# Kernel optimization log

Hardware: AMD Instinct MI355X
Metric: run time of the kernel (lower is better)

Reference implementation:

```python
import jax, jax.numpy as jnp
import numpy as np

N = 20000      # nodes (B in the original code)
T = 8          # timesteps
D_IN = 256     # in_dim (must equal hid_dim due to conv_h_n reuse in original)
D_HID = 256
D_OUT = 64
E = 320000     # edges


def setup_inputs() -> dict:
    key = jax.random.key(0)
    ks = jax.random.split(key, 18)
    s = 0.05
    w = lambda k, shape: jax.random.normal(k, shape, jnp.float32) * s
    return {
        "x": jax.random.normal(ks[0], (N, T, D_IN), jnp.float32),
        "edge_index": jax.random.randint(ks[1], (2, E), 0, N),
        "W_xr": w(ks[2], (D_IN, D_HID)),  "b_xr": w(ks[3], (D_HID,)),
        "W_hr": w(ks[4], (D_HID, D_HID)), "b_hr": w(ks[5], (D_HID,)),
        "W_xz": w(ks[6], (D_IN, D_HID)),  "b_xz": w(ks[7], (D_HID,)),
        "W_hz": w(ks[8], (D_HID, D_HID)), "b_hz": w(ks[9], (D_HID,)),
        "W_hn": w(ks[10], (D_HID, D_HID)), "b_hn": w(ks[11], (D_HID,)),
        "W_fc": w(ks[12], (D_HID, D_OUT)), "b_fc": w(ks[13], (D_OUT,)),
    }


def reference(x, edge_index, W_xr, b_xr, W_hr, b_hr, W_xz, b_xz, W_hz, b_hz,
              W_hn, b_hn, W_fc, b_fc):
    n_nodes = x.shape[0]
    src, dst = edge_index[0], edge_index[1]

    # GCN symmetric normalization with self-loops (PyG GCNConv default):
    # deg[i] = 1 + #incoming edges; norm_e = d^-1/2[src]*d^-1/2[dst]
    deg = jax.ops.segment_sum(jnp.ones(src.shape[0], x.dtype), dst,
                              num_segments=n_nodes) + jnp.asarray(1.0, x.dtype)
    dis = jax.lax.rsqrt(deg)
    enorm = dis[src] * dis[dst]      # [E]
    snorm = dis * dis                # self-loop coefficient 1/deg, [N]

    def gcn(v, W, b):
        vw = v @ W                                              # [N, D]
        agg = jax.ops.segment_sum(vw[src] * enorm[:, None], dst,
                                  num_segments=n_nodes)
        return agg + vw * snorm[:, None] + b

    def step(h, x_t):
        r = jax.nn.sigmoid(gcn(x_t, W_xr, b_xr) + gcn(h, W_hr, b_hr))
        z = jax.nn.sigmoid(gcn(x_t, W_xz, b_xz) + gcn(h, W_hz, b_hz))
        # faithful to original: conv_h_n is applied to BOTH x and h
        n = jnp.tanh(gcn(x_t, W_hn, b_hn) + r * gcn(h, W_hn, b_hn))
        h_new = (1.0 - z) * h + z * n
        return h_new, None

    h0 = jnp.zeros((n_nodes, W_hr.shape[0]), x.dtype)
    h, _ = jax.lax.scan(step, h0, jnp.transpose(x, (1, 0, 2)))  # scan over T
    return h @ W_fc + b_fc
```

## Files before the change

kernel.cpp:

```cpp
#include <hip/hip_runtime.h>
#include <hip/hip_bf16.h>
#include <math.h>

#define N_NODES 20000
#define T_STEPS 8
#define DDIM    256
#define DOUT    64
#define NE      320000
#define XSTR    2048

typedef unsigned short u16;
typedef __attribute__((ext_vector_type(8))) short  short8;
typedef __attribute__((ext_vector_type(4))) float  f32x4;

__device__ __forceinline__ float bf2f(u16 u) {
    union { unsigned int i; float f; } v; v.i = ((unsigned int)u) << 16; return v.f;
}
__device__ __forceinline__ u16 f2bf(float f) {
    union { float f; unsigned int i; } v; v.f = f;
    unsigned int r = v.i + 0x7fff + ((v.i >> 16) & 1);
    return (u16)(r >> 16);
}

__global__ void k_count(const int* __restrict__ dst, int* __restrict__ cnt) {
    int e = blockIdx.x * blockDim.x + threadIdx.x;
    if (e < NE) atomicAdd(&cnt[dst[e]], 1);
}

__global__ void k_degnorm(const int* __restrict__ cnt, float* __restrict__ dis,
                          float* __restrict__ snorm) {
    int n = blockIdx.x * blockDim.x + threadIdx.x;
    if (n < N_NODES) {
        float deg = (float)(cnt[n] + 1);
        dis[n]   = rsqrtf(deg);
        snorm[n] = 1.0f / deg;
    }
}

__global__ void k_scan(const int* __restrict__ cnt, int* __restrict__ rowptr) {
    __shared__ int sums[256];
    const int CH = (N_NODES + 255) / 256;
    int t = threadIdx.x;
    int beg = t * CH;
    int end = beg + CH; if (end > N_NODES) end = N_NODES;
    int s = 0;
    for (int i = beg; i < end; i++) s += cnt[i];
    sums[t] = s;
    __syncthreads();
    if (t == 0) {
        int run = 0;
        for (int i = 0; i < 256; i++) { int v = sums[i]; sums[i] = run; run += v; }
    }
    __syncthreads();
    if (beg < N_NODES) {
        int run = sums[t];
        for (int i = beg; i < end; i++) { rowptr[i] = run; run += cnt[i]; }
        if (end == N_NODES) rowptr[N_NODES] = run;
    }
}

__global__ void k_fill(const int* __restrict__ src, const int* __restrict__ dst,
                       const int* __restrict__ rowptr, int* __restrict__ cursor,
                       const float* __restrict__ dis, int* __restrict__ csr_src,
                       float* __restrict__ csr_norm) {
    int e = blockIdx.x * blockDim.x + threadIdx.x;
    if (e < NE) {
        int d = dst[e], s = src[e];
        int pos = atomicAdd(&cursor[d], 1);
        int i = rowptr[d] + pos;
        if (i < NE) {
            csr_src[i]  = s;
            csr_norm[i] = dis[s] * dis[d];
        }
    }
}

__global__ void k_pack6(const float* __restrict__ Wxr, const float* __restrict__ Wxz,
                        const float* __restrict__ Whn, const float* __restrict__ Whr,
                        const float* __restrict__ Whz, u16* __restrict__ out) {
    int i = blockIdx.x * blockDim.x + threadIdx.x;
    if (i >= 4 * 6 * 64 * 256) return;
    int k    = i & 255;
    int c    = (i >> 8) & 63;
    int tile = (i >> 14) % 6;
    int by   = i / (6 * 64 * 256);
    const float* W;
    switch (tile) {
        case 0: W = Wxr; break; case 1: W = Wxz; break; case 2: W = Whn; break;
        case 3: W = Whr; break; case 4: W = Whz; break; default: W = Whn; break;
    }
    out[i] = f2bf(W[k * DDIM + by * 64 + c]);
}
__global__ void k_packb3(const float* __restrict__ bxr, const float* __restrict__ bhr,
                         const float* __restrict__ bxz, const float* __restrict__ bhz,
                         const float* __restrict__ bhn, float* __restrict__ bout) {
    int c = blockIdx.x * blockDim.x + threadIdx.x;
    if (c < 3 * DDIM) {
        float v;
        if (c < 256)      v = bxr[c] + bhr[c];
        else if (c < 512) v = bxz[c - 256] + bhz[c - 256];
        else              v = bhn[c - 512];
        bout[c] = v;
    }
}

__global__ __launch_bounds__(256) void k_x2bf_all(const float* __restrict__ x,
                                                  u16* __restrict__ out) {
    int i = blockIdx.x * blockDim.x + threadIdx.x;
    if (i >= N_NODES * 512) return;
    size_t o = (size_t)i << 2;
    float4 v = *(const float4*)(x + o);
    ushort4 u; u.x = f2bf(v.x); u.y = f2bf(v.y); u.z = f2bf(v.z); u.w = f2bf(v.w);
    *(ushort4*)(out + o) = u;
}

__global__ __launch_bounds__(256) void k_agg_x(const u16* __restrict__ xall,
                      const int* __restrict__ rowptr, const int* __restrict__ csr_src,
                      const float* __restrict__ csr_norm, const float* __restrict__ snorm,
                      u16* __restrict__ xaall) {
    int n = blockIdx.x * 4 + (threadIdx.x >> 6);
    if (n >= N_NODES) return;
    int lane = threadIdx.x & 63;
    int c4 = lane << 2;
    float sn = snorm[n];
    float acc[8][4];
    const u16* selfp = xall + (size_t)n * XSTR + c4;
#pragma unroll
    for (int t = 0; t < 8; t++) {
        ushort4 v = *(const ushort4*)(selfp + t * DDIM);
        acc[t][0] = bf2f(v.x) * sn; acc[t][1] = bf2f(v.y) * sn;
        acc[t][2] = bf2f(v.z) * sn; acc[t][3] = bf2f(v.w) * sn;
    }
    int beg = rowptr[n], end = rowptr[n + 1];
    int i = beg;
    for (; i + 1 < end; i += 2) {
        const u16* sp0 = xall + (size_t)csr_src[i] * XSTR + c4;
        const u16* sp1 = xall + (size_t)csr_src[i + 1] * XSTR + c4;
        float w0 = csr_norm[i], w1 = csr_norm[i + 1];
        ushort4 g0[8], g1[8];
#pragma unroll
        for (int t = 0; t < 8; t++) g0[t] = *(const ushort4*)(sp0 + t * DDIM);
#pragma unroll
        for (int t = 0; t < 8; t++) g1[t] = *(const ushort4*)(sp1 + t * DDIM);
#pragma unroll
        for (int t = 0; t < 8; t++) {
            acc[t][0] = fmaf(bf2f(g0[t].x), w0, fmaf(bf2f(g1[t].x), w1, acc[t][0]));
            acc[t][1] = fmaf(bf2f(g0[t].y), w0, fmaf(bf2f(g1[t].y), w1, acc[t][1]));
            acc[t][2] = fmaf(bf2f(g0[t].z), w0, fmaf(bf2f(g1[t].z), w1, acc[t][2]));
            acc[t][3] = fmaf(bf2f(g0[t].w), w0, fmaf(bf2f(g1[t].w), w1, acc[t][3]));
        }
    }
    if (i < end) {
        const u16* sp = xall + (size_t)csr_src[i] * XSTR + c4;
        float w = csr_norm[i];
#pragma unroll
        for (int t = 0; t < 8; t++) {
            ushort4 g = *(const ushort4*)(sp + t * DDIM);
            acc[t][0] = fmaf(bf2f(g.x), w, acc[t][0]);
            acc[t][1] = fmaf(bf2f(g.y), w, acc[t][1]);
            acc[t][2] = fmaf(bf2f(g.z), w, acc[t][2]);
            acc[t][3] = fmaf(bf2f(g.w), w, acc[t][3]);
        }
    }
    u16* op = xaall + (size_t)n * XSTR + c4;
#pragma unroll
    for (int t = 0; t < 8; t++) {
        ushort4 o;
        o.x = f2bf(acc[t][0]); o.y = f2bf(acc[t][1]);
        o.z = f2bf(acc[t][2]); o.w = f2bf(acc[t][3]);
        *(ushort4*)(op + t * DDIM) = o;
    }
}

__global__ __launch_bounds__(256) void k_agg_bf(const u16* __restrict__ in,
                      const int* __restrict__ rowptr, const int* __restrict__ csr_src,
                      const float* __restrict__ csr_norm, const float* __restrict__ snorm,
                      u16* __restrict__ out) {
    int n = blockIdx.x * 4 + (threadIdx.x >> 6);
    if (n >= N_NODES) return;
    int lane = threadIdx.x & 63;
    int c4 = lane << 2;
    float sn = snorm[n];
    ushort4 v = *(const ushort4*)(in + (size_t)n * DDIM + c4);
    float a0 = bf2f(v.x) * sn, a1 = bf2f(v.y) * sn, a2 = bf2f(v.z) * sn, a3 = bf2f(v.w) * sn;
    int beg = rowptr[n], end = rowptr[n + 1];
    int i = beg;
    for (; i + 1 < end; i += 2) {
        ushort4 g0 = *(const ushort4*)(in + (size_t)csr_src[i] * DDIM + c4);
        ushort4 g1 = *(const ushort4*)(in + (size_t)csr_src[i + 1] * DDIM + c4);
        float w0 = csr_norm[i], w1 = csr_norm[i + 1];
        a0 = fmaf(bf2f(g0.x), w0, fmaf(bf2f(g1.x), w1, a0));
        a1 = fmaf(bf2f(g0.y), w0, fmaf(bf2f(g1.y), w1, a1));
        a2 = fmaf(bf2f(g0.z), w0, fmaf(bf2f(g1.z), w1, a2));
        a3 = fmaf(bf2f(g0.w), w0, fmaf(bf2f(g1.w), w1, a3));
    }
    if (i < end) {
        ushort4 g = *(const ushort4*)(in + (size_t)csr_src[i] * DDIM + c4);
        float w = csr_norm[i];
        a0 = fmaf(bf2f(g.x), w, a0); a1 = fmaf(bf2f(g.y), w, a1);
        a2 = fmaf(bf2f(g.z), w, a2); a3 = fmaf(bf2f(g.w), w, a3);
    }
    ushort4 o; o.x = f2bf(a0); o.y = f2bf(a1); o.z = f2bf(a2); o.w = f2bf(a3);
    *(ushort4*)(out + (size_t)n * DDIM + c4) = o;
}

__device__ __forceinline__ float sigm(float x) { return 1.0f / (1.0f + expf(-x)); }

__global__ __launch_bounds__(256) void k_gate_gru(const u16* __restrict__ xa, int ldax,
        const u16* __restrict__ ha, const u16* __restrict__ BTpack,
        const float* __restrict__ bias3, float* __restrict__ h, u16* __restrict__ hbf,
        int M) {
    __shared__ u16 Axs[64 * 32];
    __shared__ u16 Ahs[64 * 32];
    __shared__ u16 Bs[6 * 64 * 32];
    int tid = threadIdx.x;
    int w = tid >> 6, lane = tid & 63;
    int rowBase = blockIdx.x * 64;
    int by = blockIdx.y;

    int srow  = lane >> 2;
    int chunk = (lane & 3) ^ ((lane >> 3) & 3);
    int sege  = chunk * 8;
    int arow = rowBase + w * 16 + srow;
    if (arow > M - 1) arow = M - 1;
    size_t xoff = (size_t)arow * ldax + sege;
    size_t hoff = (size_t)arow * DDIM + sege;
    u16* ldsAx = &Axs[w * 16 * 32];
    u16* ldsAh = &Ahs[w * 16 * 32];
    const u16* Bbase = BTpack + (size_t)by * (6 * 64 * 256);

    f32x4 ar[2][2], az[2][2], anx[2][2], anh[2][2];
#pragma unroll
    for (int m = 0; m < 2; m++)
#pragma unroll
        for (int n = 0; n < 2; n++) {
            ar[m][n] = (f32x4){0.f,0.f,0.f,0.f}; az[m][n] = (f32x4){0.f,0.f,0.f,0.f};
            anx[m][n] = (f32x4){0.f,0.f,0.f,0.f}; anh[m][n] = (f32x4){0.f,0.f,0.f,0.f};
        }

    int kq = lane >> 4, lr = lane & 15;
    int kqs = (kq ^ ((lr >> 1) & 3)) << 3;

    for (int k0 = 0; k0 < DDIM; k0 += 32) {
        __builtin_amdgcn_global_load_lds(
            (const __attribute__((address_space(1))) void*)(xa + xoff + k0),
            (__attribute__((address_space(3))) void*)ldsAx, 16, 0, 0);
        __builtin_amdgcn_global_load_lds(
            (const __attribute__((address_space(1))) void*)(ha + hoff + k0),
            (__attribute__((address_space(3))) void*)ldsAh, 16, 0, 0);
#pragma unroll
        for (int j6 = 0; j6 < 6; j6++) {
            int j = w * 6 + j6;
            int tile = j >> 2, q = j & 3;
            const u16* src = Bbase + ((size_t)tile * 64 + q * 16 + srow) * 256 + k0 + sege;
            u16* dst = &Bs[tile * 2048 + q * 512];
            __builtin_amdgcn_global_load_lds(
                (const __attribute__((address_space(1))) void*)src,
                (__attribute__((address_space(3))) void*)dst, 16, 0, 0);
        }
        __syncthreads();

        short8 ax[2], ah[2], bf[6][2];
#pragma unroll
        for (int m = 0; m < 2; m++) {
            int r = (w >> 1) * 32 + m * 16 + lr;
            ax[m] = *(const short8*)&Axs[r * 32 + kqs];
            ah[m] = *(const short8*)&Ahs[r * 32 + kqs];
        }
#pragma unroll
        for (int t = 0; t < 6; t++)
#pragma unroll
            for (int n = 0; n < 2; n++) {
                int c = (w & 1) * 32 + n * 16 + lr;
                bf[t][n] = *(const short8*)&Bs[t * 2048 + c * 32 + kqs];
            }
#pragma unroll
        for (int m = 0; m < 2; m++)
#pragma unroll
            for (int n = 0; n < 2; n++) {
                ar[m][n]  = __builtin_amdgcn_mfma_f32_16x16x32_bf16(ax[m], bf[0][n], ar[m][n], 0, 0, 0);
                ar[m][n]  = __builtin_amdgcn_mfma_f32_16x16x32_bf16(ah[m], bf[3][n], ar[m][n], 0, 0, 0);
                az[m][n]  = __builtin_amdgcn_mfma_f32_16x16x32_bf16(ax[m], bf[1][n], az[m][n], 0, 0, 0);
                az[m][n]  = __builtin_amdgcn_mfma_f32_16x16x32_bf16(ah[m], bf[4][n], az[m][n], 0, 0, 0);
                anx[m][n] = __builtin_amdgcn_mfma_f32_16x16x32_bf16(ax[m], bf[2][n], anx[m][n], 0, 0, 0);
                anh[m][n] = __builtin_amdgcn_mfma_f32_16x16x32_bf16(ah[m], bf[5][n], anh[m][n], 0, 0, 0);
            }
        __syncthreads();
    }

#pragma unroll
    for (int n = 0; n < 2; n++) {
        int col = by * 64 + (w & 1) * 32 + n * 16 + lr;
        float br = bias3[col], bz = bias3[256 + col], bn = bias3[512 + col];
#pragma unroll
        for (int m = 0; m < 2; m++) {
            int row0 = rowBase + (w >> 1) * 32 + m * 16 + kq * 4;
#pragma unroll
            for (int j = 0; j < 4; j++) {
                int row = row0 + j;
                if (row < M) {
                    float r = sigm(ar[m][n][j] + br);
                    float z = sigm(az[m][n][j] + bz);
                    float nn = tanhf(anx[m][n][j] + bn + r * (anh[m][n][j] + bn));
                    size_t idx = (size_t)row * DDIM + col;
                    float hv = h[idx];
                    hv = (1.0f - z) * hv + z * nn;
                    h[idx] = hv;
                    hbf[idx] = f2bf(hv);
                }
            }
        }
    }
}

__global__ __launch_bounds__(256) void k_gemm(const float* __restrict__ A,
        const float* __restrict__ B, const float* __restrict__ bias,
        float* __restrict__ C, int M, int N, int K) {
    __shared__ float Asm[16][132];
    __shared__ float Bsm[16][128];
    int tid = threadIdx.x;
    int tx = tid & 15, ty = tid >> 4;
    int rowBase = blockIdx.x * 128;
    int colBase = blockIdx.y * 128;

    float acc[8][8];
#pragma unroll
    for (int i = 0; i < 8; i++)
#pragma unroll
        for (int j = 0; j < 8; j++) acc[i][j] = 0.0f;

    int arow = tid >> 1;
    int acol = (tid & 1) * 8;
    int brow = tid >> 4;
    int bcol = (tid & 15) * 8;

    bool avalid = (rowBase + arow) < M;
    const float* Aptr = A + (size_t)(rowBase + arow) * K + acol;
    int bc = colBase + bcol;
    bool bvalid = bc < N;

    for (int k0 = 0; k0 < K; k0 += 16) {
        float4 a0 = {0,0,0,0}, a1 = {0,0,0,0};
        if (avalid) {
            a0 = *(const float4*)(Aptr + k0);
            a1 = *(const float4*)(Aptr + k0 + 4);
        }
        Asm[acol + 0][arow] = a0.x; Asm[acol + 1][arow] = a0.y;
        Asm[acol + 2][arow] = a0.z; Asm[acol + 3][arow] = a0.w;
        Asm[acol + 4][arow] = a1.x; Asm[acol + 5][arow] = a1.y;
        Asm[acol + 6][arow] = a1.z; Asm[acol + 7][arow] = a1.w;

        float4 b0 = {0,0,0,0}, b1 = {0,0,0,0};
        if (bvalid) {
            const float* Bp = B + (size_t)(k0 + brow) * N + bc;
            b0 = *(const float4*)(Bp);
            b1 = *(const float4*)(Bp + 4);
        }
        *(float4*)&Bsm[brow][bcol]     = b0;
        *(float4*)&Bsm[brow][bcol + 4] = b1;
        __syncthreads();

#pragma unroll
        for (int k = 0; k < 16; k++) {
            float a[8], b[8];
            *(float4*)&a[0] = *(const float4*)&Asm[k][ty * 8];
            *(float4*)&a[4] = *(const float4*)&Asm[k][ty * 8 + 4];
            *(float4*)&b[0] = *(const float4*)&Bsm[k][tx * 8];
            *(float4*)&b[4] = *(const float4*)&Bsm[k][tx * 8 + 4];
#pragma unroll
            for (int i = 0; i < 8; i++)
#pragma unroll
                for (int j = 0; j < 8; j++)
                    acc[i][j] = fmaf(a[i], b[j], acc[i][j]);
        }
        __syncthreads();
    }

    int c0 = colBase + tx * 8;
    if (c0 < N) {
        float4 bia0 = *(const float4*)(bias + c0);
        float4 bia1 = *(const float4*)(bias + c0 + 4);
#pragma unroll
        for (int i = 0; i < 8; i++) {
            int r = rowBase + ty * 8 + i;
            if (r < M) {
                float4 o0, o1;
                o0.x = acc[i][0] + bia0.x; o0.y = acc[i][1] + bia0.y;
                o0.z = acc[i][2] + bia0.z; o0.w = acc[i][3] + bia0.w;
                o1.x = acc[i][4] + bia1.x; o1.y = acc[i][5] + bia1.y;
                o1.z = acc[i][6] + bia1.z; o1.w = acc[i][7] + bia1.w;
                *(float4*)(C + (size_t)r * N + c0)     = o0;
                *(float4*)(C + (size_t)r * N + c0 + 4) = o1;
            }
        }
    }
}

extern "C" void kernel_launch(void* const* d_in, const int* in_sizes, int n_in,
                              void* d_out, int out_size, void* d_ws, size_t ws_size,
                              hipStream_t stream) {
    const float* x    = (const float*)d_in[0];
    const int*   eidx = (const int*)d_in[1];
    const int*   src  = eidx;
    const int*   dst  = eidx + NE;
    const float* W_xr = (const float*)d_in[2];  const float* b_xr = (const float*)d_in[3];
    const float* W_hr = (const float*)d_in[4];  const float* b_hr = (const float*)d_in[5];
    const float* W_xz = (const float*)d_in[6];  const float* b_xz = (const float*)d_in[7];
    const float* W_hz = (const float*)d_in[8];  const float* b_hz = (const float*)d_in[9];
    const float* W_hn = (const float*)d_in[10]; const float* b_hn = (const float*)d_in[11];
    const float* W_fc = (const float*)d_in[12]; const float* b_fc = (const float*)d_in[13];
    float* out = (float*)d_out;

    char* ws = (char*)d_ws;
    size_t off = 0;
    auto alloc = [&](size_t bytes) -> char* {
        char* p = ws + off;
        off += (bytes + 255) & ~(size_t)255;
        return p;
    };
    const size_t NB  = (size_t)N_NODES * DDIM * 4;
    const size_t NBH = (size_t)N_NODES * DDIM * 2;
    u16*   xall    = (u16*)alloc((size_t)N_NODES * XSTR * 2);
    u16*   xaall   = (u16*)alloc((size_t)N_NODES * XSTR * 2);
    float* h       = (float*)alloc(NB);
    u16*   hbf     = (u16*)alloc(NBH);
    u16*   ha      = (u16*)alloc(NBH);
    u16*   BTpack  = (u16*)alloc((size_t)4 * 6 * 64 * 256 * 2);
    float* bias3   = (float*)alloc(3 * DDIM * 4);
    int*   cnt     = (int*)alloc(N_NODES * 4);
    int*   cursor  = (int*)alloc(N_NODES * 4);
    int*   rowptr  = (int*)alloc((N_NODES + 1) * 4);
    int*   csr_src = (int*)alloc(NE * 4);
    float* csr_nrm = (float*)alloc(NE * 4);
    float* dis     = (float*)alloc(N_NODES * 4);
    float* snorm   = (float*)alloc(N_NODES * 4);

    hipMemsetAsync(cnt, 0, N_NODES * 4, stream);
    hipMemsetAsync(cursor, 0, N_NODES * 4, stream);
    hipMemsetAsync(h, 0, NB, stream);
    hipMemsetAsync(hbf, 0, NBH, stream);

    const int TB = 256;
    k_count<<<(NE + TB - 1) / TB, TB, 0, stream>>>(dst, cnt);
    k_degnorm<<<(N_NODES + TB - 1) / TB, TB, 0, stream>>>(cnt, dis, snorm);
    k_scan<<<1, 256, 0, stream>>>(cnt, rowptr);
    k_fill<<<(NE + TB - 1) / TB, TB, 0, stream>>>(src, dst, rowptr, cursor, dis,
                                                  csr_src, csr_nrm);
    k_pack6<<<(4 * 6 * 64 * 256 + TB - 1) / TB, TB, 0, stream>>>(W_xr, W_xz, W_hn,
                                                                 W_hr, W_hz, BTpack);
    k_packb3<<<(3 * DDIM + TB - 1) / TB, TB, 0, stream>>>(b_xr, b_hr, b_xz, b_hz,
                                                          b_hn, bias3);

    k_x2bf_all<<<(N_NODES * 512 + TB - 1) / TB, TB, 0, stream>>>(x, xall);
    int aggGrid = (N_NODES + 3) / 4;
    k_agg_x<<<aggGrid, TB, 0, stream>>>(xall, rowptr, csr_src, csr_nrm, snorm, xaall);

    dim3 gGate((N_NODES + 63) / 64, 4);
    dim3 gfc((N_NODES + 127) / 128, 1);

    for (int t = 0; t < T_STEPS; t++) {
        k_agg_bf<<<aggGrid, TB, 0, stream>>>(hbf, rowptr, csr_src, csr_nrm, snorm, ha);
        k_gate_gru<<<gGate, TB, 0, stream>>>(xaall + t * DDIM, XSTR, ha, BTpack,
                                             bias3, h, hbf, N_NODES);
    }
    k_gemm<<<gfc, TB, 0, stream>>>(h, W_fc, b_fc, out, N_NODES, DOUT, DDIM);
}
```

Before: 1.216 ms.

## Hoist input-side gate GEMMs out of the time loop into one batched GEMM

```diff
diff --git a/kernel.cpp b/kernel.cpp
--- a/kernel.cpp
+++ b/kernel.cpp
@@ -8,6 +8,7 @@
 #define DOUT    64
 #define NE      320000
 #define XSTR    2048
+#define MROWS   (N_NODES * T_STEPS)
 
 typedef unsigned short u16;
 typedef __attribute__((ext_vector_type(8))) short  short8;
@@ -75,27 +76,23 @@
     }
 }
 
-__global__ void k_pack6(const float* __restrict__ Wxr, const float* __restrict__ Wxz,
-                        const float* __restrict__ Whn, const float* __restrict__ Whr,
-                        const float* __restrict__ Whz, u16* __restrict__ out) {
+__global__ void k_pack3T(const float* __restrict__ Wa, const float* __restrict__ Wb,
+                         const float* __restrict__ Wc, u16* __restrict__ out) {
     int i = blockIdx.x * blockDim.x + threadIdx.x;
-    if (i >= 4 * 6 * 64 * 256) return;
-    int k    = i & 255;
-    int c    = (i >> 8) & 63;
-    int tile = (i >> 14) % 6;
-    int by   = i / (6 * 64 * 256);
-    const float* W;
-    switch (tile) {
-        case 0: W = Wxr; break; case 1: W = Wxz; break; case 2: W = Whn; break;
-        case 3: W = Whr; break; case 4: W = Whz; break; default: W = Whn; break;
-    }
-    out[i] = f2bf(W[k * DDIM + by * 64 + c]);
+    if (i < 768 * DDIM) {
+        int c = i >> 8, k = i & 255;
+        float v;
+        if (c < 256)      v = Wa[k * DDIM + c];
+        else if (c < 512) v = Wb[k * DDIM + (c - 256)];
+        else              v = Wc[k * DDIM + (c - 512)];
+        out[i] = f2bf(v);
+    }
 }
 __global__ void k_packb3(const float* __restrict__ bxr, const float* __restrict__ bhr,
                          const float* __restrict__ bxz, const float* __restrict__ bhz,
                          const float* __restrict__ bhn, float* __restrict__ bout) {
     int c = blockIdx.x * blockDim.x + threadIdx.x;
-    if (c < 3 * DDIM) {
+    if (c < 768) {
         float v;
         if (c < 256)      v = bxr[c] + bhr[c];
         else if (c < 512) v = bxz[c - 256] + bhz[c - 256];
@@ -182,11 +179,12 @@
     int c4 = lane << 2;
     float sn = snorm[n];
     ushort4 v = *(const ushort4*)(in + (size_t)n * DDIM + c4);
-    float a0 = bf2f(v.x) * sn, a1 = bf2f(v.y) * sn, a2 = bf2f(v.z) * sn, a3 = bf2f(v.w) * sn;
+    float a0 = bf2f(v.x) * sn, a1 = bf2f(v.y) * sn;
+    float a2 = bf2f(v.z) * sn, a3 = bf2f(v.w) * sn;
     int beg = rowptr[n], end = rowptr[n + 1];
     int i = beg;
     for (; i + 1 < end; i += 2) {
-        ushort4 g0 = *(const ushort4*)(in + (size_t)csr_src[i] * DDIM + c4);
+        ushort4 g0 = *(const ushort4*)(in + (size_t)csr_src[i]     * DDIM + c4);
         ushort4 g1 = *(const ushort4*)(in + (size_t)csr_src[i + 1] * DDIM + c4);
         float w0 = csr_norm[i], w1 = csr_norm[i + 1];
         a0 = fmaf(bf2f(g0.x), w0, fmaf(bf2f(g1.x), w1, a0));
@@ -204,17 +202,103 @@
     *(ushort4*)(out + (size_t)n * DDIM + c4) = o;
 }
 
-__device__ __forceinline__ float sigm(float x) { return 1.0f / (1.0f + expf(-x)); }
-
-__global__ __launch_bounds__(256) void k_gate_gru(const u16* __restrict__ xa, int ldax,
-        const u16* __restrict__ ha, const u16* __restrict__ BTpack,
-        const float* __restrict__ bias3, float* __restrict__ h, u16* __restrict__ hbf,
-        int M) {
-    __shared__ u16 Axs[64 * 32];
-    __shared__ u16 Ahs[64 * 32];
-    __shared__ u16 Bs[6 * 64 * 32];
+__global__ __launch_bounds__(256) void k_gemm_x(const u16* __restrict__ A,
+        const u16* __restrict__ BT, const float* __restrict__ bias3,
+        u16* __restrict__ Grz, float* __restrict__ Gnx) {
+    __shared__ u16 Af[8 * 128 * 32];
+    __shared__ u16 Bs[128 * 32];
     int tid = threadIdx.x;
     int w = tid >> 6, lane = tid & 63;
+    int wr = w >> 1, wc = w & 1;
+    int rowBase = blockIdx.x * 128;
+
+    int srow  = lane >> 2;
+    int chunk = (lane & 3) ^ ((lane >> 3) & 3);
+    int sege  = chunk * 8;
+
+#pragma unroll
+    for (int i = 0; i < 16; i++) {
+        int kg = i >> 1;
+        int rg = w * 2 + (i & 1);
+        const u16* srcp = A + (size_t)(rowBase + rg * 16 + srow) * DDIM + kg * 32 + sege;
+        u16* dstp = &Af[kg * 4096 + rg * 512];
+        __builtin_amdgcn_global_load_lds(
+            (const __attribute__((address_space(1))) void*)srcp,
+            (__attribute__((address_space(3))) void*)dstp, 16, 0, 0);
+    }
+    __syncthreads();
+
+    int kq = lane >> 4, lr = lane & 15;
+    int kqs = (kq ^ ((lr >> 1) & 3)) << 3;
+
+    f32x4 acc[4][4];
+#pragma unroll
+    for (int m = 0; m < 4; m++)
+#pragma unroll
+        for (int n = 0; n < 4; n++) acc[m][n] = (f32x4){0.f, 0.f, 0.f, 0.f};
+
+    for (int j = 0; j < 48; j++) {
+        int cy = j >> 3, kg = j & 7;
+        __syncthreads();
+#pragma unroll
+        for (int i = 0; i < 2; i++) {
+            int cg = w * 2 + i;
+            const u16* srcp = BT + (size_t)(cy * 128 + cg * 16 + srow) * DDIM
+                                 + kg * 32 + sege;
+            u16* dstp = &Bs[cg * 512];
+            __builtin_amdgcn_global_load_lds(
+                (const __attribute__((address_space(1))) void*)srcp,
+                (__attribute__((address_space(3))) void*)dstp, 16, 0, 0);
+        }
+        __syncthreads();
+
+        short8 af[4], bf[4];
+#pragma unroll
+        for (int m = 0; m < 4; m++)
+            af[m] = *(const short8*)&Af[kg * 4096 + (wr * 64 + m * 16 + lr) * 32 + kqs];
+#pragma unroll
+        for (int n = 0; n < 4; n++)
+            bf[n] = *(const short8*)&Bs[(wc * 64 + n * 16 + lr) * 32 + kqs];
+#pragma unroll
+        for (int m = 0; m < 4; m++)
+#pragma unroll
+            for (int n = 0; n < 4; n++)
+                acc[m][n] = __builtin_amdgcn_mfma_f32_16x16x32_bf16(
+                    af[m], bf[n], acc[m][n], 0, 0, 0);
+
+        if (kg == 7) {
+#pragma unroll
+            for (int n = 0; n < 4; n++) {
+                int gc = cy * 128 + wc * 64 + n * 16 + lr;
+                float bv = bias3[gc];
+#pragma unroll
+                for (int m = 0; m < 4; m++) {
+                    int row0 = rowBase + wr * 64 + m * 16 + kq * 4;
+#pragma unroll
+                    for (int jj = 0; jj < 4; jj++) {
+                        int row = row0 + jj;
+                        float v = acc[m][n][jj] + bv;
+                        if (cy < 4) Grz[(size_t)row * 512 + gc] = f2bf(v);
+                        else        Gnx[(size_t)row * 256 + (gc - 512)] = v;
+                        acc[m][n][jj] = 0.0f;
+                    }
+                }
+            }
+        }
+    }
+}
+
+__device__ __forceinline__ float sigm(float x) { return 1.0f / (1.0f + expf(-x)); }
+
+__global__ __launch_bounds__(256) void k_gruh(const u16* __restrict__ ha,
+        const u16* __restrict__ WhT3, const u16* __restrict__ Grz,
+        const float* __restrict__ Gnx, const float* __restrict__ bias3, int t,
+        float* __restrict__ h, u16* __restrict__ hbf, int M) {
+    __shared__ u16 Ahs[64 * 32];
+    __shared__ u16 Bs[3 * 64 * 32];
+    int tid = threadIdx.x;
+    int w = tid >> 6, lane = tid & 63;
+    int wr = w >> 1, wc = w & 1;
     int rowBase = blockIdx.x * 64;
     int by = blockIdx.y;
 
@@ -223,85 +307,74 @@
     int sege  = chunk * 8;
     int arow = rowBase + w * 16 + srow;
     if (arow > M - 1) arow = M - 1;
-    size_t xoff = (size_t)arow * ldax + sege;
     size_t hoff = (size_t)arow * DDIM + sege;
-    u16* ldsAx = &Axs[w * 16 * 32];
-    u16* ldsAh = &Ahs[w * 16 * 32];
-    const u16* Bbase = BTpack + (size_t)by * (6 * 64 * 256);
-
-    f32x4 ar[2][2], az[2][2], anx[2][2], anh[2][2];
+    u16* ldsAh = &Ahs[w * 512];
+
+    f32x4 arh[2][2], azh[2][2], anh[2][2];
 #pragma unroll
     for (int m = 0; m < 2; m++)
 #pragma unroll
         for (int n = 0; n < 2; n++) {
-            ar[m][n] = (f32x4){0.f,0.f,0.f,0.f}; az[m][n] = (f32x4){0.f,0.f,0.f,0.f};
-            anx[m][n] = (f32x4){0.f,0.f,0.f,0.f}; anh[m][n] = (f32x4){0.f,0.f,0.f,0.f};
+            arh[m][n] = (f32x4){0.f,0.f,0.f,0.f};
+            azh[m][n] = (f32x4){0.f,0.f,0.f,0.f};
+            anh[m][n] = (f32x4){0.f,0.f,0.f,0.f};
         }
 
     int kq = lane >> 4, lr = lane & 15;
     int kqs = (kq ^ ((lr >> 1) & 3)) << 3;
 
     for (int k0 = 0; k0 < DDIM; k0 += 32) {
-        __builtin_amdgcn_global_load_lds(
-            (const __attribute__((address_space(1))) void*)(xa + xoff + k0),
-            (__attribute__((address_space(3))) void*)ldsAx, 16, 0, 0);
         __builtin_amdgcn_global_load_lds(
             (const __attribute__((address_space(1))) void*)(ha + hoff + k0),
             (__attribute__((address_space(3))) void*)ldsAh, 16, 0, 0);
 #pragma unroll
-        for (int j6 = 0; j6 < 6; j6++) {
-            int j = w * 6 + j6;
-            int tile = j >> 2, q = j & 3;
-            const u16* src = Bbase + ((size_t)tile * 64 + q * 16 + srow) * 256 + k0 + sege;
-            u16* dst = &Bs[tile * 2048 + q * 512];
+        for (int i = 0; i < 3; i++) {
+            int seg = w * 3 + i;
+            int tile = seg >> 2, q = seg & 3;
+            const u16* srcp = WhT3 + (size_t)(tile * 256 + by * 64 + q * 16 + srow) * DDIM
+                                   + k0 + sege;
+            u16* dstp = &Bs[tile * 2048 + q * 512];
             __builtin_amdgcn_global_load_lds(
-                (const __attribute__((address_space(1))) void*)src,
-                (__attribute__((address_space(3))) void*)dst, 16, 0, 0);
+                (const __attribute__((address_space(1))) void*)srcp,
+                (__attribute__((address_space(3))) void*)dstp, 16, 0, 0);
         }
         __syncthreads();
 
-        short8 ax[2], ah[2], bf[6][2];
-#pragma unroll
-        for (int m = 0; m < 2; m++) {
-            int r = (w >> 1) * 32 + m * 16 + lr;
-            ax[m] = *(const short8*)&Axs[r * 32 + kqs];
-            ah[m] = *(const short8*)&Ahs[r * 32 + kqs];
-        }
-#pragma unroll
-        for (int t = 0; t < 6; t++)
+        short8 ah[2], bf[3][2];
+#pragma unroll
+        for (int m = 0; m < 2; m++)
+            ah[m] = *(const short8*)&Ahs[(wr * 32 + m * 16 + lr) * 32 + kqs];
+#pragma unroll
+        for (int g = 0; g < 3; g++)
+#pragma unroll
+            for (int n = 0; n < 2; n++)
+                bf[g][n] = *(const short8*)&Bs[g * 2048 + (wc * 32 + n * 16 + lr) * 32 + kqs];
+#pragma unroll
+        for (int m = 0; m < 2; m++)
 #pragma unroll
             for (int n = 0; n < 2; n++) {
-                int c = (w & 1) * 32 + n * 16 + lr;
-                bf[t][n] = *(const short8*)&Bs[t * 2048 + c * 32 + kqs];
-            }
-#pragma unroll
-        for (int m = 0; m < 2; m++)
-#pragma unroll
-            for (int n = 0; n < 2; n++) {
-                ar[m][n]  = __builtin_amdgcn_mfma_f32_16x16x32_bf16(ax[m], bf[0][n], ar[m][n], 0, 0, 0);
-                ar[m][n]  = __builtin_amdgcn_mfma_f32_16x16x32_bf16(ah[m], bf[3][n], ar[m][n], 0, 0, 0);
-                az[m][n]  = __builtin_amdgcn_mfma_f32_16x16x32_bf16(ax[m], bf[1][n], az[m][n], 0, 0, 0);
-                az[m][n]  = __builtin_amdgcn_mfma_f32_16x16x32_bf16(ah[m], bf[4][n], az[m][n], 0, 0, 0);
-                anx[m][n] = __builtin_amdgcn_mfma_f32_16x16x32_bf16(ax[m], bf[2][n], anx[m][n], 0, 0, 0);
-                anh[m][n] = __builtin_amdgcn_mfma_f32_16x16x32_bf16(ah[m], bf[5][n], anh[m][n], 0, 0, 0);
+                arh[m][n] = __builtin_amdgcn_mfma_f32_16x16x32_bf16(ah[m], bf[0][n], arh[m][n], 0, 0, 0);
+                azh[m][n] = __builtin_amdgcn_mfma_f32_16x16x32_bf16(ah[m], bf[1][n], azh[m][n], 0, 0, 0);
+                anh[m][n] = __builtin_amdgcn_mfma_f32_16x16x32_bf16(ah[m], bf[2][n], anh[m][n], 0, 0, 0);
             }
         __syncthreads();
     }
 
 #pragma unroll
     for (int n = 0; n < 2; n++) {
-        int col = by * 64 + (w & 1) * 32 + n * 16 + lr;
-        float br = bias3[col], bz = bias3[256 + col], bn = bias3[512 + col];
+        int col = by * 64 + wc * 32 + n * 16 + lr;
+        float bn = bias3[512 + col];
 #pragma unroll
         for (int m = 0; m < 2; m++) {
-            int row0 = rowBase + (w >> 1) * 32 + m * 16 + kq * 4;
+            int row0 = rowBase + wr * 32 + m * 16 + kq * 4;
 #pragma unroll
             for (int j = 0; j < 4; j++) {
                 int row = row0 + j;
                 if (row < M) {
-                    float r = sigm(ar[m][n][j] + br);
-                    float z = sigm(az[m][n][j] + bz);
-                    float nn = tanhf(anx[m][n][j] + bn + r * (anh[m][n][j] + bn));
+                    size_t rn = (size_t)row * 8 + t;
+                    float r = sigm(bf2f(Grz[rn * 512 + col])       + arh[m][n][j]);
+                    float z = sigm(bf2f(Grz[rn * 512 + 256 + col]) + azh[m][n][j]);
+                    float nn = tanhf(Gnx[rn * 256 + col] + r * (anh[m][n][j] + bn));
                     size_t idx = (size_t)row * DDIM + col;
                     float hv = h[idx];
                     hv = (1.0f - z) * hv + z * nn;
@@ -422,11 +495,14 @@
     const size_t NBH = (size_t)N_NODES * DDIM * 2;
     u16*   xall    = (u16*)alloc((size_t)N_NODES * XSTR * 2);
     u16*   xaall   = (u16*)alloc((size_t)N_NODES * XSTR * 2);
+    u16*   Grz     = (u16*)alloc((size_t)MROWS * 512 * 2);
+    float* Gnx     = (float*)alloc((size_t)MROWS * 256 * 4);
     float* h       = (float*)alloc(NB);
     u16*   hbf     = (u16*)alloc(NBH);
     u16*   ha      = (u16*)alloc(NBH);
-    u16*   BTpack  = (u16*)alloc((size_t)4 * 6 * 64 * 256 * 2);
-    float* bias3   = (float*)alloc(3 * DDIM * 4);
+    u16*   WxT3    = (u16*)alloc((size_t)768 * DDIM * 2);
+    u16*   WhT3    = (u16*)alloc((size_t)768 * DDIM * 2);
+    float* bias3   = (float*)alloc(768 * 4);
     int*   cnt     = (int*)alloc(N_NODES * 4);
     int*   cursor  = (int*)alloc(N_NODES * 4);
     int*   rowptr  = (int*)alloc((N_NODES + 1) * 4);
@@ -446,22 +522,22 @@
     k_scan<<<1, 256, 0, stream>>>(cnt, rowptr);
     k_fill<<<(NE + TB - 1) / TB, TB, 0, stream>>>(src, dst, rowptr, cursor, dis,
                                                   csr_src, csr_nrm);
-    k_pack6<<<(4 * 6 * 64 * 256 + TB - 1) / TB, TB, 0, stream>>>(W_xr, W_xz, W_hn,
-                                                                 W_hr, W_hz, BTpack);
-    k_packb3<<<(3 * DDIM + TB - 1) / TB, TB, 0, stream>>>(b_xr, b_hr, b_xz, b_hz,
-                                                          b_hn, bias3);
+    k_pack3T<<<(768 * DDIM + TB - 1) / TB, TB, 0, stream>>>(W_xr, W_xz, W_hn, WxT3);
+    k_pack3T<<<(768 * DDIM + TB - 1) / TB, TB, 0, stream>>>(W_hr, W_hz, W_hn, WhT3);
+    k_packb3<<<(768 + TB - 1) / TB, TB, 0, stream>>>(b_xr, b_hr, b_xz, b_hz,
+                                                     b_hn, bias3);
 
     k_x2bf_all<<<(N_NODES * 512 + TB - 1) / TB, TB, 0, stream>>>(x, xall);
     int aggGrid = (N_NODES + 3) / 4;
     k_agg_x<<<aggGrid, TB, 0, stream>>>(xall, rowptr, csr_src, csr_nrm, snorm, xaall);
-
-    dim3 gGate((N_NODES + 63) / 64, 4);
+    k_gemm_x<<<MROWS / 128, TB, 0, stream>>>(xaall, WxT3, bias3, Grz, Gnx);
+
+    dim3 gGru((N_NODES + 63) / 64, 4);
     dim3 gfc((N_NODES + 127) / 128, 1);
 
     for (int t = 0; t < T_STEPS; t++) {
         k_agg_bf<<<aggGrid, TB, 0, stream>>>(hbf, rowptr, csr_src, csr_nrm, snorm, ha);
-        k_gate_gru<<<gGate, TB, 0, stream>>>(xaall + t * DDIM, XSTR, ha, BTpack,
-                                             bias3, h, hbf, N_NODES);
+        k_gruh<<<gGru, TB, 0, stream>>>(ha, WhT3, Grz, Gnx, bias3, t, h, hbf, N_NODES);
     }
     k_gemm<<<gfc, TB, 0, stream>>>(h, W_fc, b_fc, out, N_NODES, DOUT, DDIM);
 }
```

New measurement: 1.404 ms. +15.5%, slower.
